# Kernel tuning notes

Measured on AMD Instinct MI355X. Metric: run time of the kernel, lower is better.

Reference implementation:

```python
import jax, jax.numpy as jnp
import numpy as np

B, S, E, H = 2, 2048, 1024, 16
DH = E // H  # 64


def setup_inputs() -> dict:
    key = jax.random.key(0)
    ks = jax.random.split(key, 9)
    sc = 1.0 / np.sqrt(E)
    return {
        "x": jax.random.normal(ks[0], (B, S, E), dtype=jnp.float32),
        "Wq": jax.random.normal(ks[1], (E, E), dtype=jnp.float32) * sc,
        "bq": jax.random.normal(ks[2], (E,), dtype=jnp.float32) * 0.02,
        "Wk": jax.random.normal(ks[3], (E, E), dtype=jnp.float32) * sc,
        "bk": jax.random.normal(ks[4], (E,), dtype=jnp.float32) * 0.02,
        "Wv": jax.random.normal(ks[5], (E, E), dtype=jnp.float32) * sc,
        "bv": jax.random.normal(ks[6], (E,), dtype=jnp.float32) * 0.02,
        "Wo": jax.random.normal(ks[7], (E, E), dtype=jnp.float32) * sc,
        "bo": jax.random.normal(ks[8], (E,), dtype=jnp.float32) * 0.02,
    }


def reference(x, Wq, bq, Wk, bk, Wv, bv, Wo, bo):
    b, s, e = x.shape
    h, dh = H, e // H
    # NOTE: original torch code does .view(B, H, S, Dh) on the [B, S, E]
    # projection WITHOUT transposing first; we replicate that exact reshape.
    q = (x @ Wq.T + bq).reshape(b, h, s, dh)
    k = (x @ Wk.T + bk).reshape(b, h, s, dh)
    v = (x @ Wv.T + bv).reshape(b, h, s, dh)
    scale = 1.0 / jnp.sqrt(jnp.asarray(dh, dtype=x.dtype))
    scores = jax.nn.softmax(jnp.einsum("bhqd,bhkd->bhqk", q, k) * scale, axis=-1)
    out = jnp.einsum("bhqk,bhkd->bhqd", scores, v)  # [B,H,S,Dh]
    out = out.transpose(0, 2, 1, 3).reshape(b, s, e)  # matches torch transpose(1,2).view
    return out @ Wo.T + bo
```

## Files before the change

kernel.cpp:

```cpp
#include <hip/hip_runtime.h>
#include <hip/hip_bf16.h>
#include <stdint.h>

typedef __bf16 bf16x8 __attribute__((ext_vector_type(8)));
typedef float  f32x4  __attribute__((ext_vector_type(4)));
typedef float  f32x16 __attribute__((ext_vector_type(16)));
typedef __hip_bfloat16 bf16;

__device__ __forceinline__ void gll16(const void* g, void* l) {
    typedef const unsigned int __attribute__((address_space(1)))* gp_t;
    typedef unsigned int __attribute__((address_space(3)))* lp_t;
    __builtin_amdgcn_global_load_lds((gp_t)(g), (lp_t)(l), 16, 0, 0);
}

__global__ __launch_bounds__(256) void prep_convert(
    const float* __restrict__ x,
    const float* __restrict__ wq, const float* __restrict__ wk,
    const float* __restrict__ wv, const float* __restrict__ wo,
    bf16* __restrict__ Xb, bf16* __restrict__ Wcat, bf16* __restrict__ Wob)
{
    int i = blockIdx.x * blockDim.x + threadIdx.x;
    int base = i * 4;
    const float* src; bf16* dst;
    if      (base < 4194304) { src = x  + base;             dst = Xb   + base; }
    else if (base < 5242880) { src = wq + (base - 4194304); dst = Wcat + (base - 4194304); }
    else if (base < 6291456) { src = wk + (base - 5242880); dst = Wcat + 1048576 + (base - 5242880); }
    else if (base < 7340032) { src = wv + (base - 6291456); dst = Wcat + 2097152 + (base - 6291456); }
    else                     { src = wo + (base - 7340032); dst = Wob  + (base - 7340032); }
    float4 v = *(const float4*)src;
    union { bf16 h[4]; ushort4 u; } cv;
    cv.h[0] = __float2bfloat16(v.x);
    cv.h[1] = __float2bfloat16(v.y);
    cv.h[2] = __float2bfloat16(v.z);
    cv.h[3] = __float2bfloat16(v.w);
    *(ushort4*)dst = cv.u;
}

__global__ __launch_bounds__(256, 2) void gemm_qkv(
    const bf16* __restrict__ X, const bf16* __restrict__ Wc,
    const float* __restrict__ bq, const float* __restrict__ bk, const float* __restrict__ bv,
    bf16* __restrict__ Pq, bf16* __restrict__ Pk, bf16* __restrict__ Pv)
{
    __shared__ __align__(16) bf16 Ab[128 * 32];
    __shared__ __align__(16) bf16 Bb[128 * 32];
    const int t = threadIdx.x;
    const int lane = t & 63, w = t >> 6;
    const int lr = lane & 15, lg = lane >> 4;
    const int wr = w >> 1, wc = w & 1;
    const int row0 = blockIdx.y * 128, col0 = blockIdx.x * 128;

    f32x4 acc[4][4] = {};

    const char* Xc  = (const char*)X;
    const char* Wcc = (const char*)Wc;
    char* AbC = (char*)Ab;
    char* BbC = (char*)Bb;
    const int o0 = t * 16, o1 = o0 + 4096;
    const int ldsoff = w * 1024;

    for (int k0 = 0; k0 < 1024; k0 += 32) {
        __syncthreads();
        gll16(Xc  + (size_t)(row0 + (o0 >> 6)) * 2048 + (size_t)k0 * 2 + (o0 & 63), AbC + ldsoff);
        gll16(Wcc + (size_t)(col0 + (o0 >> 6)) * 2048 + (size_t)k0 * 2 + (o0 & 63), BbC + ldsoff);
        gll16(Xc  + (size_t)(row0 + (o1 >> 6)) * 2048 + (size_t)k0 * 2 + (o1 & 63), AbC + 4096 + ldsoff);
        gll16(Wcc + (size_t)(col0 + (o1 >> 6)) * 2048 + (size_t)k0 * 2 + (o1 & 63), BbC + 4096 + ldsoff);
        __syncthreads();
        bf16x8 af[4], bw[4];
        #pragma unroll
        for (int i = 0; i < 4; ++i)
            af[i] = *(const bf16x8*)(AbC + ((wr * 64 + i * 16 + lr) * 32 + lg * 8) * 2);
        #pragma unroll
        for (int j = 0; j < 4; ++j)
            bw[j] = *(const bf16x8*)(BbC + ((wc * 64 + j * 16 + lr) * 32 + lg * 8) * 2);
        #pragma unroll
        for (int i = 0; i < 4; ++i)
            #pragma unroll
            for (int j = 0; j < 4; ++j)
                acc[i][j] = __builtin_amdgcn_mfma_f32_16x16x32_bf16(af[i], bw[j], acc[i][j], 0, 0, 0);
    }

    const int mid = col0 >> 10;
    const float* bias = (mid == 0) ? bq : (mid == 1 ? bk : bv);
    bf16* Out = (mid == 0) ? Pq : (mid == 1 ? Pk : Pv);
    const float scale = (mid == 0) ? 0.125f * 1.44269504f : 1.0f;
    const int nc0 = col0 - (mid << 10) + wc * 64;
    const int mr0 = row0 + wr * 64;
    #pragma unroll
    for (int i = 0; i < 4; ++i)
        #pragma unroll
        for (int j = 0; j < 4; ++j) {
            int cc = nc0 + j * 16 + lr;
            float bsv = bias[cc];
            #pragma unroll
            for (int p = 0; p < 4; ++p) {
                int rr = mr0 + i * 16 + lg * 4 + p;
                Out[(size_t)rr * 1024 + cc] = __float2bfloat16((acc[i][j][p] + bsv) * scale);
            }
        }
}

__global__ __launch_bounds__(256) void transpose_v(const bf16* __restrict__ Pv, bf16* __restrict__ Vt)
{
    __shared__ bf16 tile[64][72];
    const int head = blockIdx.y;
    const int st   = blockIdx.x;
    const bf16* src = Pv + (size_t)head * 131072 + (size_t)st * 4096;
    bf16* dst = Vt + (size_t)head * 131072 + (size_t)st * 64;
    const int t = threadIdx.x;
    const int rr = t >> 2, c0 = (t & 3) * 16;
    #pragma unroll
    for (int u = 0; u < 2; ++u) {
        bf16x8 v = *(const bf16x8*)(src + rr * 64 + c0 + u * 8);
        #pragma unroll
        for (int e = 0; e < 8; ++e) tile[rr][c0 + u * 8 + e] = ((const bf16*)&v)[e];
    }
    __syncthreads();
    #pragma unroll
    for (int u = 0; u < 2; ++u) {
        bf16 ov[8];
        #pragma unroll
        for (int e = 0; e < 8; ++e) {
            int y = u * 8 + e;
            int z = (y & 3) | ((y & 8) >> 1) | ((y & 4) << 1);
            ov[e] = tile[c0 + z][rr];
        }
        *(bf16x8*)(dst + (size_t)rr * 2048 + c0 + u * 8) = *(const bf16x8*)ov;
    }
}

__global__ __launch_bounds__(256, 2) void attn_fwd(
    const bf16* __restrict__ Pq, const bf16* __restrict__ Pk,
    const bf16* __restrict__ Vt, bf16* __restrict__ Of)
{
    __shared__ __align__(16) bf16 Kl[128 * 64];
    __shared__ __align__(16) bf16 Vl[64 * 128];

    const int blk = blockIdx.x;
    const int head = blk >> 4;
    const int qt = blk & 15;
    const int bb = head >> 4, hh = head & 15;
    const bf16* Qh = Pq + (size_t)head * 131072;
    const char* Khc = (const char*)(Pk + (size_t)head * 131072);
    const char* Vhc = (const char*)(Vt + (size_t)head * 131072);

    const int t = threadIdx.x;
    const int lane = t & 63, w = t >> 6;
    const int ql = lane & 31, hi = lane >> 5;
    const int q0 = qt * 128 + w * 32;

    char* KlC = (char*)Kl;
    char* VlC = (char*)Vl;

    bf16x8 qf[4];
    #pragma unroll
    for (int m = 0; m < 4; ++m)
        qf[m] = *(const bf16x8*)(Qh + (size_t)(q0 + ql) * 64 + m * 16 + hi * 8);

    f32x16 acc[2] = {};
    float m_run = -1e30f, l_run = 0.f;

    for (int s0 = 0; s0 < 2048; s0 += 128) {
        __syncthreads();
        #pragma unroll
        for (int qq = 0; qq < 4; ++qq) {
            int o = qq * 4096 + t * 16;
            int key = o >> 7, ks = (o >> 4) & 7;
            gll16(Khc + (size_t)(s0 + key) * 128 + ((ks ^ (key & 7)) * 16), KlC + qq * 4096 + w * 1024);
            int d = o >> 8, vs = (o >> 4) & 15;
            gll16(Vhc + (size_t)d * 4096 + (size_t)s0 * 2 + ((vs ^ (d & 7)) * 16), VlC + qq * 4096 + w * 1024);
        }
        __syncthreads();

        f32x16 sa[4] = {};
        #pragma unroll
        for (int kb = 0; kb < 4; ++kb) {
            int row = kb * 32 + ql;
            #pragma unroll
            for (int m = 0; m < 4; ++m) {
                int byt = row * 128 + ((32 * m + 16 * hi) ^ ((row & 7) << 4));
                bf16x8 kf = *(const bf16x8*)(KlC + byt);
                sa[kb] = __builtin_amdgcn_mfma_f32_32x32x16_bf16(kf, qf[m], sa[kb], 0, 0, 0);
            }
        }

        float mx = -1e30f;
        #pragma unroll
        for (int kb = 0; kb < 4; ++kb)
            #pragma unroll
            for (int r = 0; r < 16; ++r) mx = fmaxf(mx, sa[kb][r]);
        mx = fmaxf(mx, __shfl_xor(mx, 32));
        float mn = fmaxf(m_run, mx);
        float al = exp2f(m_run - mn);
        m_run = mn;
        float rs = 0.f;
        #pragma unroll
        for (int kb = 0; kb < 4; ++kb)
            #pragma unroll
            for (int r = 0; r < 16; ++r) {
                float p = exp2f(sa[kb][r] - mn);
                sa[kb][r] = p;
                rs += p;
            }
        rs += __shfl_xor(rs, 32);
        l_run = l_run * al + rs;
        #pragma unroll
        for (int r = 0; r < 16; ++r) { acc[0][r] *= al; acc[1][r] *= al; }

        #pragma unroll
        for (int sb = 0; sb < 8; ++sb) {
            const int kb = sb >> 1, par = (sb & 1) * 8;
            bf16x8 pa;
            #pragma unroll
            for (int e = 0; e < 8; ++e) pa[e] = (__bf16)sa[kb][par + e];
            #pragma unroll
            for (int db = 0; db < 2; ++db) {
                int row = db * 32 + ql;
                int byt = row * 256 + ((sb * 32 + hi * 16) ^ ((row & 7) << 4));
                bf16x8 vf = *(const bf16x8*)(VlC + byt);
                acc[db] = __builtin_amdgcn_mfma_f32_32x32x16_bf16(vf, pa, acc[db], 0, 0, 0);
            }
        }
    }

    float inv = 1.0f / l_run;
    bf16* orow = Of + (size_t)(bb * 2048 + q0 + ql) * 1024 + hh * 64;
    #pragma unroll
    for (int db = 0; db < 2; ++db)
        #pragma unroll
        for (int g = 0; g < 4; ++g) {
            union { bf16 h[4]; ushort4 u; } ob;
            #pragma unroll
            for (int j = 0; j < 4; ++j)
                ob.h[j] = __float2bfloat16(acc[db][4 * g + j] * inv);
            *(ushort4*)(orow + db * 32 + 8 * g + 4 * hi) = ob.u;
        }
}

__global__ __launch_bounds__(256, 2) void gemm_out(
    const bf16* __restrict__ A, const bf16* __restrict__ W,
    const float* __restrict__ bo, float* __restrict__ C)
{
    __shared__ __align__(16) bf16 Ab[128 * 32];
    __shared__ __align__(16) bf16 Bb[128 * 32];
    const int t = threadIdx.x;
    const int lane = t & 63, w = t >> 6;
    const int lr = lane & 15, lg = lane >> 4;
    const int wr = w >> 1, wc = w & 1;
    const int row0 = blockIdx.y * 128, col0 = blockIdx.x * 128;

    f32x4 acc[4][4] = {};
    const char* Ac = (const char*)A;
    const char* Wc = (const char*)W;
    char* AbC = (char*)Ab;
    char* BbC = (char*)Bb;
    const int o0 = t * 16, o1 = o0 + 4096;
    const int ldsoff = w * 1024;

    for (int k0 = 0; k0 < 1024; k0 += 32) {
        __syncthreads();
        gll16(Ac + (size_t)(row0 + (o0 >> 6)) * 2048 + (size_t)k0 * 2 + (o0 & 63), AbC + ldsoff);
        gll16(Wc + (size_t)(col0 + (o0 >> 6)) * 2048 + (size_t)k0 * 2 + (o0 & 63), BbC + ldsoff);
        gll16(Ac + (size_t)(row0 + (o1 >> 6)) * 2048 + (size_t)k0 * 2 + (o1 & 63), AbC + 4096 + ldsoff);
        gll16(Wc + (size_t)(col0 + (o1 >> 6)) * 2048 + (size_t)k0 * 2 + (o1 & 63), BbC + 4096 + ldsoff);
        __syncthreads();
        bf16x8 af[4], bw[4];
        #pragma unroll
        for (int i = 0; i < 4; ++i)
            af[i] = *(const bf16x8*)(AbC + ((wr * 64 + i * 16 + lr) * 32 + lg * 8) * 2);
        #pragma unroll
        for (int j = 0; j < 4; ++j)
            bw[j] = *(const bf16x8*)(BbC + ((wc * 64 + j * 16 + lr) * 32 + lg * 8) * 2);
        #pragma unroll
        for (int i = 0; i < 4; ++i)
            #pragma unroll
            for (int j = 0; j < 4; ++j)
                acc[i][j] = __builtin_amdgcn_mfma_f32_16x16x32_bf16(af[i], bw[j], acc[i][j], 0, 0, 0);
    }

    const int nc0 = col0 + wc * 64;
    const int mr0 = row0 + wr * 64;
    #pragma unroll
    for (int i = 0; i < 4; ++i)
        #pragma unroll
        for (int j = 0; j < 4; ++j) {
            int cc = nc0 + j * 16 + lr;
            float bsv = bo[cc];
            #pragma unroll
            for (int p = 0; p < 4; ++p) {
                int rr = mr0 + i * 16 + lg * 4 + p;
                C[(size_t)rr * 1024 + cc] = acc[i][j][p] + bsv;
            }
        }
}

extern "C" void kernel_launch(void* const* d_in, const int* in_sizes, int n_in,
                              void* d_out, int out_size, void* d_ws, size_t ws_size,
                              hipStream_t stream) {
    const float* x  = (const float*)d_in[0];
    const float* Wq = (const float*)d_in[1];
    const float* bq = (const float*)d_in[2];
    const float* Wk = (const float*)d_in[3];
    const float* bk = (const float*)d_in[4];
    const float* Wv = (const float*)d_in[5];
    const float* bv = (const float*)d_in[6];
    const float* Wo = (const float*)d_in[7];
    const float* bo = (const float*)d_in[8];
    float* out = (float*)d_out;

    char* ws = (char*)d_ws;
    bf16* Xb   = (bf16*)(ws + 0);
    bf16* Wcat = (bf16*)(ws + 8388608);
    bf16* Wob  = (bf16*)(ws + 14680064);
    bf16* Pq   = (bf16*)(ws + 16777216);
    bf16* Pk   = (bf16*)(ws + 25165824);
    bf16* Pv   = (bf16*)(ws + 33554432);
    bf16* Vt   = (bf16*)(ws + 0);
    bf16* Of   = (bf16*)(ws + 33554432);
    (void)ws_size; (void)in_sizes; (void)n_in; (void)out_size;

    prep_convert<<<8192, 256, 0, stream>>>(x, Wq, Wk, Wv, Wo, Xb, Wcat, Wob);
    gemm_qkv<<<dim3(24, 32), 256, 0, stream>>>(Xb, Wcat, bq, bk, bv, Pq, Pk, Pv);
    transpose_v<<<dim3(32, 32), 256, 0, stream>>>(Pv, Vt);
    attn_fwd<<<512, 256, 0, stream>>>(Pq, Pk, Vt, Of);
    gemm_out<<<dim3(8, 32), 256, 0, stream>>>(Of, Wob, bo, out);
}
```

Measured before the change: 137.0 us.

## Double-buffer K/V tiles in attention, add MFMA priority and native exp2

Splits the attention kernel's K and V shared-memory tiles into two buffers and prefetches the next 128-key tile while the current one is computed, cutting one barrier per iteration. It also raises wave priority around the MFMA loops and replaces exp2f with the hardware v_exp_f32 instruction. Shared memory per block doubles to 64KB, which may limit how many blocks fit per CU at launch_bounds(256,2). The async global_load_lds into the other buffer relies on the trailing barrier for correctness.

```diff
diff --git a/kernel.cpp b/kernel.cpp
--- a/kernel.cpp
+++ b/kernel.cpp
@@ -11,6 +11,14 @@
     typedef const unsigned int __attribute__((address_space(1)))* gp_t;
     typedef unsigned int __attribute__((address_space(3)))* lp_t;
     __builtin_amdgcn_global_load_lds((gp_t)(g), (lp_t)(l), 16, 0, 0);
+}
+
+__device__ __forceinline__ float fexp2(float x) {
+#if __has_builtin(__builtin_amdgcn_exp2f)
+    return __builtin_amdgcn_exp2f(x);
+#else
+    float r; asm volatile("v_exp_f32 %0, %1" : "=v"(r) : "v"(x)); return r;
+#endif
 }
 
 __global__ __launch_bounds__(256) void prep_convert(
@@ -132,8 +140,8 @@
     const bf16* __restrict__ Pq, const bf16* __restrict__ Pk,
     const bf16* __restrict__ Vt, bf16* __restrict__ Of)
 {
-    __shared__ __align__(16) bf16 Kl[128 * 64];
-    __shared__ __align__(16) bf16 Vl[64 * 128];
+    __shared__ __align__(16) bf16 Kl[2][128 * 64];
+    __shared__ __align__(16) bf16 Vl[2][64 * 128];
 
     const int blk = blockIdx.x;
     const int head = blk >> 4;
@@ -148,9 +156,6 @@
     const int ql = lane & 31, hi = lane >> 5;
     const int q0 = qt * 128 + w * 32;
 
-    char* KlC = (char*)Kl;
-    char* VlC = (char*)Vl;
-
     bf16x8 qf[4];
     #pragma unroll
     for (int m = 0; m < 4; ++m)
@@ -159,19 +164,38 @@
     f32x16 acc[2] = {};
     float m_run = -1e30f, l_run = 0.f;
 
+    const int stg_o   = t * 16;
+    const int stg_key = stg_o >> 7, stg_ks = (stg_o >> 4) & 7;
+    const int stg_d   = stg_o >> 8, stg_vs = (stg_o >> 4) & 15;
+    const size_t kgo = (size_t)stg_key * 128 + ((stg_ks ^ (stg_key & 7)) * 16);
+    const size_t vgo = (size_t)stg_d * 4096 + ((stg_vs ^ (stg_d & 7)) * 16);
+    const int ldst = w * 1024;
+
+#define STAGE(S0, BUF)                                                          \
+    {                                                                           \
+        char* KB = (char*)(Kl[BUF]);                                            \
+        char* VB = (char*)(Vl[BUF]);                                            \
+        _Pragma("unroll")                                                       \
+        for (int qq = 0; qq < 4; ++qq) {                                        \
+            gll16(Khc + (size_t)(S0) * 128 + (size_t)qq * 4096 + kgo,           \
+                  KB + qq * 4096 + ldst);                                       \
+            gll16(Vhc + (size_t)(S0) * 2 + (size_t)qq * 65536 + vgo,            \
+                  VB + qq * 4096 + ldst);                                       \
+        }                                                                       \
+    }
+
+    STAGE(0, 0);
+    __syncthreads();
+
+    int cur = 0;
     for (int s0 = 0; s0 < 2048; s0 += 128) {
-        __syncthreads();
-        #pragma unroll
-        for (int qq = 0; qq < 4; ++qq) {
-            int o = qq * 4096 + t * 16;
-            int key = o >> 7, ks = (o >> 4) & 7;
-            gll16(Khc + (size_t)(s0 + key) * 128 + ((ks ^ (key & 7)) * 16), KlC + qq * 4096 + w * 1024);
-            int d = o >> 8, vs = (o >> 4) & 15;
-            gll16(Vhc + (size_t)d * 4096 + (size_t)s0 * 2 + ((vs ^ (d & 7)) * 16), VlC + qq * 4096 + w * 1024);
-        }
-        __syncthreads();
+        if (s0 + 128 < 2048) STAGE(s0 + 128, cur ^ 1);
+
+        const char* KlC = (const char*)(Kl[cur]);
+        const char* VlC = (const char*)(Vl[cur]);
 
         f32x16 sa[4] = {};
+        __builtin_amdgcn_s_setprio(1);
         #pragma unroll
         for (int kb = 0; kb < 4; ++kb) {
             int row = kb * 32 + ql;
@@ -182,6 +206,7 @@
                 sa[kb] = __builtin_amdgcn_mfma_f32_32x32x16_bf16(kf, qf[m], sa[kb], 0, 0, 0);
             }
         }
+        __builtin_amdgcn_s_setprio(0);
 
         float mx = -1e30f;
         #pragma unroll
@@ -190,14 +215,14 @@
             for (int r = 0; r < 16; ++r) mx = fmaxf(mx, sa[kb][r]);
         mx = fmaxf(mx, __shfl_xor(mx, 32));
         float mn = fmaxf(m_run, mx);
-        float al = exp2f(m_run - mn);
+        float al = fexp2(m_run - mn);
         m_run = mn;
         float rs = 0.f;
         #pragma unroll
         for (int kb = 0; kb < 4; ++kb)
             #pragma unroll
             for (int r = 0; r < 16; ++r) {
-                float p = exp2f(sa[kb][r] - mn);
+                float p = fexp2(sa[kb][r] - mn);
                 sa[kb][r] = p;
                 rs += p;
             }
@@ -206,6 +231,7 @@
         #pragma unroll
         for (int r = 0; r < 16; ++r) { acc[0][r] *= al; acc[1][r] *= al; }
 
+        __builtin_amdgcn_s_setprio(1);
         #pragma unroll
         for (int sb = 0; sb < 8; ++sb) {
             const int kb = sb >> 1, par = (sb & 1) * 8;
@@ -220,7 +246,12 @@
                 acc[db] = __builtin_amdgcn_mfma_f32_32x32x16_bf16(vf, pa, acc[db], 0, 0, 0);
             }
         }
-    }
+        __builtin_amdgcn_s_setprio(0);
+
+        __syncthreads();
+        cur ^= 1;
+    }
+#undef STAGE
 
     float inv = 1.0f / l_run;
     bf16* orow = Of + (size_t)(bb * 2048 + q0 + ql) * 1024 + hh * 64;
```

Measured after the change: 125.8 us. 8.2% less time.
